# Optimization experiments

Hardware: AMD Instinct MI355X
Metric: run time of the kernel (lower is better)

## Reference

```python
import jax, jax.numpy as jnp
import numpy as np

C = 512      # filters
G = 32       # groups
EPS = 1e-6

def setup_inputs() -> dict:
    key = jax.random.key(0)
    ks = jax.random.split(key, 10)
    B, H, W = 2, 64, 64
    inputs = jax.random.normal(ks[0], (B, H, W, C), dtype=jnp.float32)
    scale = 1.0 / np.sqrt(C)
    def w(k):
        return jax.random.normal(k, (C, C), dtype=jnp.float32) * scale
    return {
        "inputs": inputs,
        "gn_gamma": jnp.ones((C,), jnp.float32),
        "gn_beta": jnp.zeros((C,), jnp.float32),
        "wq": w(ks[1]), "bq": jnp.zeros((C,), jnp.float32),
        "wk": w(ks[2]), "bk": jnp.zeros((C,), jnp.float32),
        "wv": w(ks[3]), "bv": jnp.zeros((C,), jnp.float32),
        "wo": w(ks[4]), "bo": jnp.zeros((C,), jnp.float32),
    }

def _group_norm(x, gamma, beta):
    B, H, W, c = x.shape
    xg = x.reshape(B, H, W, G, c // G)
    mean = jnp.mean(xg, axis=(1, 2, 4), keepdims=True)
    var = jnp.var(xg, axis=(1, 2, 4), keepdims=True)
    xg = (xg - mean) * jax.lax.rsqrt(var + EPS)
    return xg.reshape(B, H, W, c) * gamma + beta

def reference(inputs, gn_gamma, gn_beta, wq, bq, wk, bk, wv, bv, wo, bo):
    B, H, W, c = inputs.shape
    x = _group_norm(inputs, gn_gamma, gn_beta)
    # 1x1 convs == per-pixel linear layers
    q = (x @ wq + bq).reshape(B, H * W, c)
    k = (x @ wk + bk).reshape(B, H * W, c)
    v = (x @ wv + bv).reshape(B, H * W, c)
    q = q * jnp.asarray(1.0 / np.sqrt(float(c)), q.dtype)
    scores = jnp.einsum('bnc,bmc->bnm', q, k).astype(jnp.float32)  # [B,N,N]
    probs = jax.nn.softmax(scores, axis=-1).astype(inputs.dtype)
    attn = jnp.einsum('bnm,bmc->bnc', probs, v)
    out = attn.reshape(B, H, W, c) @ wo + bo
    return out + inputs
```

## Files before the change

### kernel.cpp

```cpp
#include <hip/hip_runtime.h>
#include <math.h>

typedef __bf16 bf16;
typedef __bf16 bf16x8 __attribute__((ext_vector_type(8)));
typedef float  f32x4  __attribute__((ext_vector_type(4)));

#define DEV __device__ __forceinline__
#define VMCNT(n) asm volatile("s_waitcnt vmcnt(" #n ")" ::: "memory")
#define CFENCE  asm volatile("" ::: "memory")
#define BAR()   { CFENCE; __builtin_amdgcn_s_barrier(); CFENCE; }

DEV void gload_lds16(const bf16* g, bf16* l) {
  __builtin_amdgcn_global_load_lds(
      (const __attribute__((address_space(1))) void*)g,
      (__attribute__((address_space(3))) void*)l, 16, 0, 0);
}

#define OFF_STATS 0UL
#define OFF_WOT   1024UL
#define OFF_BIASQ 525312UL
#define OFF_WTQKV 531456UL
#define OFF_XN    2104320UL
#define OFF_QKV   10492928UL
#define OFF_VT    35658752UL
#define OFF_S     44047360UL
#define OFF_INVL  111156224UL
#define OFF_P0    2104320UL
#define OFF_P1    18881536UL
#define OFF_ATTN  44047360UL
#define OFF_GNP   44047360UL

__global__ __launch_bounds__(256) void gn_part_k(const float* __restrict__ x,
                                                 float2* __restrict__ part) {
  const int blk = blockIdx.x;
  const int chunk = blk & 15;
  const int bg = blk >> 4;
  const int b = bg >> 5, g = bg & 31;
  const int t = threadIdx.x;
  const int p = chunk * 256 + t;
  const float* xp = x + (size_t)b * (4096 * 512) + (size_t)p * 512 + g * 16;
  float4 v0 = *(const float4*)(xp);
  float4 v1 = *(const float4*)(xp + 4);
  float4 v2 = *(const float4*)(xp + 8);
  float4 v3 = *(const float4*)(xp + 12);
  float s  = v0.x + v0.y + v0.z + v0.w + v1.x + v1.y + v1.z + v1.w
           + v2.x + v2.y + v2.z + v2.w + v3.x + v3.y + v3.z + v3.w;
  float ss = v0.x*v0.x + v0.y*v0.y + v0.z*v0.z + v0.w*v0.w
           + v1.x*v1.x + v1.y*v1.y + v1.z*v1.z + v1.w*v1.w
           + v2.x*v2.x + v2.y*v2.y + v2.z*v2.z + v2.w*v2.w
           + v3.x*v3.x + v3.y*v3.y + v3.z*v3.z + v3.w*v3.w;
#pragma unroll
  for (int off = 32; off; off >>= 1) {
    s  += __shfl_xor(s, off);
    ss += __shfl_xor(ss, off);
  }
  __shared__ float rs[4], rss[4];
  const int w = t >> 6, l = t & 63;
  if (l == 0) { rs[w] = s; rss[w] = ss; }
  __syncthreads();
  if (t == 0)
    part[blk] = make_float2(rs[0] + rs[1] + rs[2] + rs[3],
                            rss[0] + rss[1] + rss[2] + rss[3]);
}

__global__ void gn_finish_k(const float2* __restrict__ part,
                            float2* __restrict__ stats) {
  const int g = threadIdx.x;
  float s = 0.f, ss = 0.f;
#pragma unroll
  for (int c = 0; c < 16; ++c) {
    float2 p = part[g * 16 + c];
    s += p.x; ss += p.y;
  }
  float mean = s * (1.0f / 65536.0f);
  float var  = ss * (1.0f / 65536.0f) - mean * mean;
  stats[g] = make_float2(mean, 1.0f / sqrtf(var + 1e-6f));
}

__global__ __launch_bounds__(256) void gn_apply_k(const float* __restrict__ x,
                                                  const float2* __restrict__ stats,
                                                  const float* __restrict__ gamma,
                                                  const float* __restrict__ beta,
                                                  bf16* __restrict__ xn) {
  size_t i = ((size_t)blockIdx.x * 256 + threadIdx.x) * 8;
  const int c = (int)(i & 511);
  const int b = (int)(i >> 21);
  float2 st = stats[b * 32 + (c >> 4)];
  float4 xa = *(const float4*)(x + i);
  float4 xb = *(const float4*)(x + i + 4);
  float4 ga = *(const float4*)(gamma + c);
  float4 gb = *(const float4*)(gamma + c + 4);
  float4 ba = *(const float4*)(beta + c);
  float4 bb = *(const float4*)(beta + c + 4);
  bf16x8 o;
  o[0] = (bf16)((xa.x - st.x) * st.y * ga.x + ba.x);
  o[1] = (bf16)((xa.y - st.x) * st.y * ga.y + ba.y);
  o[2] = (bf16)((xa.z - st.x) * st.y * ga.z + ba.z);
  o[3] = (bf16)((xa.w - st.x) * st.y * ga.w + ba.w);
  o[4] = (bf16)((xb.x - st.x) * st.y * gb.x + bb.x);
  o[5] = (bf16)((xb.y - st.x) * st.y * gb.y + bb.y);
  o[6] = (bf16)((xb.z - st.x) * st.y * gb.z + bb.z);
  o[7] = (bf16)((xb.w - st.x) * st.y * gb.w + bb.w);
  *(bf16x8*)(xn + i) = o;
}

__global__ void prep_w_k(const float* __restrict__ wq, const float* __restrict__ wk,
                         const float* __restrict__ wv, const float* __restrict__ wo,
                         bf16* __restrict__ wt_qkv, bf16* __restrict__ wot, float qscale) {
  const int z = blockIdx.z;
  const float* W = (z == 0) ? wq : (z == 1) ? wk : (z == 2) ? wv : wo;
  bf16* dst = (z < 3) ? (wt_qkv + (size_t)z * 512 * 512) : wot;
  const float s = (z == 0) ? qscale : 1.0f;
  __shared__ float tile[32][33];
  const int i0 = blockIdx.y * 32;
  const int o0 = blockIdx.x * 32;
#pragma unroll
  for (int r = threadIdx.y; r < 32; r += 8)
    tile[r][threadIdx.x] = W[(size_t)(i0 + r) * 512 + o0 + threadIdx.x];
  __syncthreads();
#pragma unroll
  for (int r = threadIdx.y; r < 32; r += 8)
    dst[(size_t)(o0 + r) * 512 + i0 + threadIdx.x] = (bf16)(tile[threadIdx.x][r] * s);
}

__global__ void prep_bias_k(const float* __restrict__ bq, const float* __restrict__ bk,
                            const float* __restrict__ bv, float* __restrict__ bias_qkv,
                            float qscale) {
  int i = blockIdx.x * 256 + threadIdx.x;
  float v = (i < 512) ? bq[i] * qscale : (i < 1024) ? bk[i - 512] : bv[i - 1024];
  bias_qkv[i] = v;
}

__global__ void transpose_v_k(const bf16* __restrict__ qkv, bf16* __restrict__ vt) {
  __shared__ bf16 tile[32][33];
  const int z = blockIdx.z;
  const int n0 = blockIdx.x * 32, d0 = blockIdx.y * 32;
  const bf16* src = qkv + (size_t)z * 4096 * 1536 + 1024;
#pragma unroll
  for (int r = threadIdx.y; r < 32; r += 8)
    tile[r][threadIdx.x] = src[(size_t)(n0 + r) * 1536 + d0 + threadIdx.x];
  __syncthreads();
  bf16* dst = vt + (size_t)z * 512 * 4096;
#pragma unroll
  for (int r = threadIdx.y; r < 32; r += 8)
    dst[(size_t)(d0 + r) * 4096 + n0 + threadIdx.x] = tile[threadIdx.x][r];
}

__global__ __launch_bounds__(256) void rowsum_k(const bf16* __restrict__ S,
                                                float* __restrict__ invl) {
  const int r = blockIdx.x;
  const bf16* p = S + (size_t)r * 4096 + threadIdx.x * 16;
  bf16x8 u0 = *(const bf16x8*)p;
  bf16x8 u1 = *(const bf16x8*)(p + 8);
  float s = 0.f;
#pragma unroll
  for (int j = 0; j < 8; ++j) s += (float)u0[j] + (float)u1[j];
#pragma unroll
  for (int off = 32; off; off >>= 1) s += __shfl_xor(s, off);
  __shared__ float red[4];
  const int w = threadIdx.x >> 6, l = threadIdx.x & 63;
  if (l == 0) red[w] = s;
  __syncthreads();
  if (threadIdx.x == 0)
    invl[r] = 1.0f / (red[0] + red[1] + red[2] + red[3]);
}

__global__ __launch_bounds__(256) void reduce_pv_k(const float* __restrict__ p0,
                                                   const float* __restrict__ p1,
                                                   const float* __restrict__ invl,
                                                   bf16* __restrict__ attn) {
  size_t i = ((size_t)blockIdx.x * 256 + threadIdx.x) * 8;
  const float il = invl[i >> 9];
  float4 a = *(const float4*)(p0 + i);
  float4 b = *(const float4*)(p0 + i + 4);
  float4 c = *(const float4*)(p1 + i);
  float4 d = *(const float4*)(p1 + i + 4);
  bf16x8 o;
  o[0] = (bf16)((a.x + c.x) * il); o[1] = (bf16)((a.y + c.y) * il);
  o[2] = (bf16)((a.z + c.z) * il); o[3] = (bf16)((a.w + c.w) * il);
  o[4] = (bf16)((b.x + d.x) * il); o[5] = (bf16)((b.y + d.y) * il);
  o[6] = (bf16)((b.z + d.z) * il); o[7] = (bf16)((b.w + d.w) * il);
  *(bf16x8*)(attn + i) = o;
}

template <int BM, int BN, int EPI, int GX, int GY, int GZ>
__global__ __launch_bounds__(256, 2) void gemm_nt(
    const bf16* __restrict__ A, int lda, long sAz,
    const bf16* __restrict__ B, int ldb, long sBz,
    void* __restrict__ C, int ldc, long sCz,
    int nk,
    const float* __restrict__ bias,
    const float* __restrict__ resid) {
  constexpr int WM = BM / 2, WN = BN / 2;
  constexpr int FM = BM / 32, FN = BN / 32;
  constexpr int NWG = GX * GY * GZ;
  constexpr int CPX = NWG / 8;
  __shared__ alignas(16) bf16 As[2][BM * 64];
  __shared__ alignas(16) bf16 Bs[2][BN * 64];

  const int lin = blockIdx.x;
  const int wid = (lin & 7) * CPX + (lin >> 3);
  const int bx = wid % GX;
  const int by = (wid / GX) % GY;
  const int bz = wid / (GX * GY);

  const int t = threadIdx.x;
  const bf16* Aq = A + (size_t)bz * sAz + (size_t)by * BM * lda;
  const bf16* Bq = B + (size_t)bz * sBz + (size_t)bx * BN * ldb;

  const int srow = t >> 3;
  const int sg   = (t & 7) ^ (srow & 7);

  auto stage = [&](int buf, int kt) {
    const int k0 = kt * 64 + sg * 8;
#pragma unroll
    for (int i = 0; i < BM / 32; ++i)
      gload_lds16(Aq + (size_t)(i * 32 + srow) * lda + k0, &As[buf][i * 2048 + t * 8]);
#pragma unroll
    for (int i = 0; i < BN / 32; ++i)
      gload_lds16(Bq + (size_t)(i * 32 + srow) * ldb + k0, &Bs[buf][i * 2048 + t * 8]);
  };

  const int l = t & 63, w = t >> 6;
  const int wr = w >> 1, wc = w & 1;
  const int lr = l & 15, kh = l >> 4;
  const int rs = lr & 7;

  f32x4 acc[FM][FN] = {};

  stage(0, 0);
  for (int kt = 0; kt < nk; ++kt) {
    __syncthreads();
    if (kt + 1 < nk) stage((kt + 1) & 1, kt + 1);
    const int buf = kt & 1;
    bf16x8 a[2][FM], b[2][FN];
#pragma unroll
    for (int h = 0; h < 2; ++h) {
      const int g = ((h * 4 + kh) ^ rs) * 8;
#pragma unroll
      for (int m = 0; m < FM; ++m)
        a[h][m] = *(const bf16x8*)(&As[buf][(wr * WM + m * 16 + lr) * 64 + g]);
#pragma unroll
      for (int n = 0; n < FN; ++n)
        b[h][n] = *(const bf16x8*)(&Bs[buf][(wc * WN + n * 16 + lr) * 64 + g]);
    }
#pragma unroll
    for (int h = 0; h < 2; ++h)
#pragma unroll
      for (int m = 0; m < FM; ++m)
#pragma unroll
        for (int n = 0; n < FN; ++n)
          acc[m][n] = __builtin_amdgcn_mfma_f32_16x16x32_bf16(a[h][m], b[h][n], acc[m][n], 0, 0, 0);
  }

  const int gr0 = by * BM + wr * WM + kh * 4;
  const int gc0 = bx * BN + wc * WN + lr;
#pragma unroll
  for (int m = 0; m < FM; ++m)
#pragma unroll
    for (int n = 0; n < FN; ++n) {
      const int c = gc0 + n * 16;
      float bv = bias[c];
#pragma unroll
      for (int j = 0; j < 4; ++j) {
        const int r = gr0 + m * 16 + j;
        float val = acc[m][n][j] + bv;
        if constexpr (EPI == 2) {
          float* Cf = (float*)C + (size_t)bz * sCz;
          Cf[(size_t)r * ldc + c] = val + resid[(size_t)r * ldc + c];
        } else {
          bf16* Cb = (bf16*)C + (size_t)bz * sCz;
          Cb[(size_t)r * ldc + c] = (bf16)val;
        }
      }
    }
}

template <int BM, int BN, int WR, int WC, int EPI, int GX, int GY, int GZ, int KS>
__global__ __launch_bounds__(512, 2) void gemm_8p(
    const bf16* __restrict__ A, int lda, long sAz,
    const bf16* __restrict__ B, int ldb, long sBz,
    void* __restrict__ C0, void* __restrict__ C1, int ldc, long sCz,
    int nt) {
  constexpr int WM = BM / WR, WN = BN / WC;
  constexpr int FM = WM / 16, FN = WN / 16;
  constexpr int HM = FM / 2, HN = FN / 2;
  constexpr int LA = BM / 128, LB = BN / 128;
  constexpr int NWG = GX * KS * GY * GZ;
  constexpr int CPX = NWG / 8;
  static_assert(WR * WC == 8, "8 waves");
  static_assert(LA == 2 && (LB == 1 || LB == 2), "vmcnt literals");

  __shared__ alignas(16) bf16 As[2][BM * 64];
  __shared__ alignas(16) bf16 Bs[2][BN * 64];

  const int t = threadIdx.x;
  const int lin = blockIdx.x;
  const int wid = (lin & 7) * CPX + (lin >> 3);
  const int bx = wid % GX;
  const int ks = (wid / GX) % KS;
  const int by = (wid / (GX * KS)) % GY;
  const int bz = wid / (GX * KS * GY);

  const long kOff = (long)ks * nt * 64;
  const bf16* Aq = A + (size_t)bz * sAz + (size_t)by * BM * lda + kOff;
  const bf16* Bq = B + (size_t)bz * sBz + (size_t)bx * BN * ldb + kOff;

  const int srow = t >> 3;
  const int sgr  = (t & 7) ^ (srow & 7);

  auto stageA = [&](int buf, int tile, int half) {
    const bf16* src = Aq + (size_t)(half * (BM / 2) + srow) * lda + tile * 64 + sgr * 8;
    bf16* dst = &As[buf][(half * (BM / 2)) * 64] + t * 8;
#pragma unroll
    for (int j = 0; j < LA; ++j)
      gload_lds16(src + (size_t)(j * 64) * lda, dst + j * 4096);
  };
  auto stageB = [&](int buf, int tile, int half) {
    const bf16* src = Bq + (size_t)(half * (BN / 2) + srow) * ldb + tile * 64 + sgr * 8;
    bf16* dst = &Bs[buf][(half * (BN / 2)) * 64] + t * 8;
#pragma unroll
    for (int j = 0; j < LB; ++j)
      gload_lds16(src + (size_t)(j * 64) * ldb, dst + j * 4096);
  };

  const int l = t & 63, w = t >> 6;
  const int wr = w / WC, wc = w % WC;
  const int lr = l & 15, kh = l >> 4;
  const int rs8 = lr & 7;

  bf16x8 af[HM][2], bf_[HN][2];
  auto readA = [&](int buf, int qm) {
#pragma unroll
    for (int i = 0; i < HM; ++i)
#pragma unroll
      for (int h = 0; h < 2; ++h)
        af[i][h] = *(const bf16x8*)(
            &As[buf][(wr * WM + qm * (WM / 2) + i * 16 + lr) * 64 + (((h * 4 + kh) ^ rs8) * 8)]);
  };
  auto readB = [&](int buf, int qn) {
#pragma unroll
    for (int j = 0; j < HN; ++j)
#pragma unroll
      for (int h = 0; h < 2; ++h)
        bf_[j][h] = *(const bf16x8*)(
            &Bs[buf][(wc * WN + qn * (WN / 2) + j * 16 + lr) * 64 + (((h * 4 + kh) ^ rs8) * 8)]);
  };

  f32x4 acc[FM][FN] = {};

#define MFMAQ(QM, QN) { \
  __builtin_amdgcn_s_setprio(1); \
  _Pragma("unroll") for (int ii = 0; ii < HM; ++ii) \
  _Pragma("unroll") for (int jj = 0; jj < HN; ++jj) \
  _Pragma("unroll") for (int h = 0; h < 2; ++h) \
    acc[(QM)*HM + ii][(QN)*HN + jj] = __builtin_amdgcn_mfma_f32_16x16x32_bf16( \
        af[ii][h], bf_[jj][h], acc[(QM)*HM + ii][(QN)*HN + jj], 0, 0, 0); \
  __builtin_amdgcn_s_setprio(0); }
#define WAIT_LB() { if constexpr (LB == 1) VMCNT(1); else VMCNT(2); }

  stageA(0, 0, 0); stageA(0, 0, 1); stageB(0, 0, 0); stageB(0, 0, 1);
  WAIT_LB();
  BAR();

  const int half = nt >> 1;
  for (int i = 0; i < half; ++i) {
    const int t1 = 2 * i + 1, t2 = 2 * i + 2;
    const bool last = (i == half - 1);
    readA(0, 0); readB(0, 0);
    stageA(1, t1, 0);
    BAR();
    MFMAQ(0, 0);
    BAR();
    readA(0, 1);
    stageA(1, t1, 1);
    BAR();
    MFMAQ(1, 0);
    VMCNT(4);
    BAR();
    readB(0, 1);
    stageB(1, t1, 0);
    BAR();
    MFMAQ(1, 1);
    BAR();
    readA(0, 0);
    stageB(1, t1, 1);
    BAR();
    MFMAQ(0, 1);
    WAIT_LB();
    BAR();
    readA(1, 0); readB(1, 0);
    if (!last) stageA(0, t2, 0);
    BAR();
    MFMAQ(0, 0);
    BAR();
    readA(1, 1);
    if (!last) stageA(0, t2, 1);
    BAR();
    MFMAQ(1, 0);
    if (last) { VMCNT(0); } else { VMCNT(4); }
    BAR();
    readB(1, 1);
    if (!last) stageB(0, t2, 0);
    BAR();
    MFMAQ(1, 1);
    BAR();
    readA(1, 0);
    if (!last) stageB(0, t2, 1);
    BAR();
    MFMAQ(0, 1);
    WAIT_LB();
    BAR();
  }
#undef MFMAQ
#undef WAIT_LB

  const int gr0 = by * BM + wr * WM + kh * 4;
  const int gc0 = bx * BN + wc * WN + lr;
#pragma unroll
  for (int m = 0; m < FM; ++m)
#pragma unroll
    for (int n = 0; n < FN; ++n) {
      const int c = gc0 + n * 16;
#pragma unroll
      for (int j = 0; j < 4; ++j) {
        const int r = gr0 + m * 16 + j;
        if constexpr (EPI == 6) {
          bf16* Cb = (bf16*)C0 + (size_t)bz * sCz;
          Cb[(size_t)r * ldc + c] = (bf16)__expf(acc[m][n][j]);
        } else {
          float* Cf = (float*)(ks ? C1 : C0) + (size_t)bz * sCz;
          Cf[(size_t)r * ldc + c] = acc[m][n][j];
        }
      }
    }
}

extern "C" void kernel_launch(void* const* d_in, const int* in_sizes, int n_in,
                              void* d_out, int out_size, void* d_ws, size_t ws_size,
                              hipStream_t stream) {
  const float* x     = (const float*)d_in[0];
  const float* gamma = (const float*)d_in[1];
  const float* beta  = (const float*)d_in[2];
  const float* wq = (const float*)d_in[3];
  const float* bq = (const float*)d_in[4];
  const float* wk = (const float*)d_in[5];
  const float* bk = (const float*)d_in[6];
  const float* wv = (const float*)d_in[7];
  const float* bv = (const float*)d_in[8];
  const float* wo = (const float*)d_in[9];
  const float* bo = (const float*)d_in[10];
  float* out = (float*)d_out;
  char* ws = (char*)d_ws;

  float2* stats    = (float2*)(ws + OFF_STATS);
  bf16*   wot      = (bf16*)(ws + OFF_WOT);
  float*  bias_qkv = (float*)(ws + OFF_BIASQ);
  bf16*   wt_qkv   = (bf16*)(ws + OFF_WTQKV);
  bf16*   xn       = (bf16*)(ws + OFF_XN);
  bf16*   qkv      = (bf16*)(ws + OFF_QKV);
  bf16*   vt       = (bf16*)(ws + OFF_VT);
  bf16*   S        = (bf16*)(ws + OFF_S);
  float*  invl     = (float*)(ws + OFF_INVL);
  float*  p0       = (float*)(ws + OFF_P0);
  float*  p1       = (float*)(ws + OFF_P1);
  bf16*   attn     = (bf16*)(ws + OFF_ATTN);
  float2* gn_part  = (float2*)(ws + OFF_GNP);

  const float qscale = 0.04419417382415922f;

  prep_w_k<<<dim3(16, 16, 4), dim3(32, 8), 0, stream>>>(wq, wk, wv, wo, wt_qkv, wot, qscale);
  prep_bias_k<<<6, 256, 0, stream>>>(bq, bk, bv, bias_qkv, qscale);
  gn_part_k<<<1024, 256, 0, stream>>>(x, gn_part);
  gn_finish_k<<<1, 64, 0, stream>>>(gn_part, stats);
  gn_apply_k<<<2048, 256, 0, stream>>>(x, stats, gamma, beta, xn);

  gemm_nt<128, 128, 1, 12, 64, 1><<<768, 256, 0, stream>>>(
      xn, 512, 0, wt_qkv, 512, 0, qkv, 1536, 0, 512 / 64, bias_qkv, nullptr);

  gemm_8p<256, 256, 2, 4, 6, 16, 16, 2, 1><<<512, 512, 0, stream>>>(
      qkv, 1536, 4096L * 1536, qkv + 512, 1536, 4096L * 1536,
      S, nullptr, 4096, 4096L * 4096, 512 / 64);

  rowsum_k<<<8192, 256, 0, stream>>>(S, invl);

  transpose_v_k<<<dim3(128, 16, 2), dim3(32, 8), 0, stream>>>(qkv, vt);

  gemm_8p<256, 128, 4, 2, 3, 4, 16, 2, 2><<<256, 512, 0, stream>>>(
      S, 4096, 4096L * 4096, vt, 4096, 512L * 4096,
      p0, p1, 512, 4096L * 512, 2048 / 64);

  reduce_pv_k<<<2048, 256, 0, stream>>>(p0, p1, invl, attn);

  gemm_nt<64, 128, 2, 4, 128, 1><<<512, 256, 0, stream>>>(
      attn, 512, 0, wot, 512, 0, out, 512, 0, 512 / 64, bo, x);
}
```

Baseline: 165.1 us.

## Write V transposed from QKV GEMM epilogue and interleave 8-phase warp tiles

Splits the QKV projection into a QK GEMM and a separate V GEMM whose epilogue writes V directly in transposed layout with 4-wide bf16 stores. This removes the standalone transpose kernel and the round trip of V through global memory. It also changes the LDS read and output indexing in the 8-phase GEMM so each wave's quadrants are interleaved across block halves, which is meant to reduce LDS bank conflicts. The trade-off is one extra kernel launch and a smaller V GEMM grid that may fill the GPU poorly.

```diff
diff --git a/kernel.cpp b/kernel.cpp
--- a/kernel.cpp
+++ b/kernel.cpp
@@ -2,6 +2,7 @@
 #include <math.h>
 
 typedef __bf16 bf16;
+typedef __bf16 bf16x4 __attribute__((ext_vector_type(4)));
 typedef __bf16 bf16x8 __attribute__((ext_vector_type(8)));
 typedef float  f32x4  __attribute__((ext_vector_type(4)));
 
@@ -21,7 +22,7 @@
 #define OFF_BIASQ 525312UL
 #define OFF_WTQKV 531456UL
 #define OFF_XN    2104320UL
-#define OFF_QKV   10492928UL
+#define OFF_QK    10492928UL
 #define OFF_VT    35658752UL
 #define OFF_S     44047360UL
 #define OFF_INVL  111156224UL
@@ -131,21 +132,6 @@
   bias_qkv[i] = v;
 }
 
-__global__ void transpose_v_k(const bf16* __restrict__ qkv, bf16* __restrict__ vt) {
-  __shared__ bf16 tile[32][33];
-  const int z = blockIdx.z;
-  const int n0 = blockIdx.x * 32, d0 = blockIdx.y * 32;
-  const bf16* src = qkv + (size_t)z * 4096 * 1536 + 1024;
-#pragma unroll
-  for (int r = threadIdx.y; r < 32; r += 8)
-    tile[r][threadIdx.x] = src[(size_t)(n0 + r) * 1536 + d0 + threadIdx.x];
-  __syncthreads();
-  bf16* dst = vt + (size_t)z * 512 * 4096;
-#pragma unroll
-  for (int r = threadIdx.y; r < 32; r += 8)
-    dst[(size_t)(d0 + r) * 4096 + n0 + threadIdx.x] = tile[threadIdx.x][r];
-}
-
 __global__ __launch_bounds__(256) void rowsum_k(const bf16* __restrict__ S,
                                                 float* __restrict__ invl) {
   const int r = blockIdx.x;
@@ -261,16 +247,25 @@
     for (int n = 0; n < FN; ++n) {
       const int c = gc0 + n * 16;
       float bv = bias[c];
-#pragma unroll
-      for (int j = 0; j < 4; ++j) {
-        const int r = gr0 + m * 16 + j;
-        float val = acc[m][n][j] + bv;
-        if constexpr (EPI == 2) {
-          float* Cf = (float*)C + (size_t)bz * sCz;
-          Cf[(size_t)r * ldc + c] = val + resid[(size_t)r * ldc + c];
-        } else {
-          bf16* Cb = (bf16*)C + (size_t)bz * sCz;
-          Cb[(size_t)r * ldc + c] = (bf16)val;
+      if constexpr (EPI == 7) {
+        const int r0 = gr0 + m * 16;
+        const int z = r0 >> 12, nn = r0 & 4095;
+        bf16x4 v;
+#pragma unroll
+        for (int j = 0; j < 4; ++j) v[j] = (bf16)(acc[m][n][j] + bv);
+        *(bf16x4*)((bf16*)C + (size_t)z * (512 * 4096) + (size_t)c * 4096 + nn) = v;
+      } else {
+#pragma unroll
+        for (int j = 0; j < 4; ++j) {
+          const int r = gr0 + m * 16 + j;
+          float val = acc[m][n][j] + bv;
+          if constexpr (EPI == 2) {
+            float* Cf = (float*)C + (size_t)bz * sCz;
+            Cf[(size_t)r * ldc + c] = val + resid[(size_t)r * ldc + c];
+          } else {
+            bf16* Cb = (bf16*)C + (size_t)bz * sCz;
+            Cb[(size_t)r * ldc + c] = (bf16)val;
+          }
         }
       }
     }
@@ -336,7 +331,7 @@
 #pragma unroll
       for (int h = 0; h < 2; ++h)
         af[i][h] = *(const bf16x8*)(
-            &As[buf][(wr * WM + qm * (WM / 2) + i * 16 + lr) * 64 + (((h * 4 + kh) ^ rs8) * 8)]);
+            &As[buf][(qm * (BM / 2) + wr * (WM / 2) + i * 16 + lr) * 64 + (((h * 4 + kh) ^ rs8) * 8)]);
   };
   auto readB = [&](int buf, int qn) {
 #pragma unroll
@@ -344,7 +339,7 @@
 #pragma unroll
       for (int h = 0; h < 2; ++h)
         bf_[j][h] = *(const bf16x8*)(
-            &Bs[buf][(wc * WN + qn * (WN / 2) + j * 16 + lr) * 64 + (((h * 4 + kh) ^ rs8) * 8)]);
+            &Bs[buf][(qn * (BN / 2) + wc * (WN / 2) + j * 16 + lr) * 64 + (((h * 4 + kh) ^ rs8) * 8)]);
   };
 
   f32x4 acc[FM][FN] = {};
@@ -415,16 +410,17 @@
 #undef MFMAQ
 #undef WAIT_LB
 
-  const int gr0 = by * BM + wr * WM + kh * 4;
-  const int gc0 = bx * BN + wc * WN + lr;
+  const int gr0 = by * BM + wr * (WM / 2) + kh * 4;
+  const int gc0 = bx * BN + wc * (WN / 2) + lr;
 #pragma unroll
   for (int m = 0; m < FM; ++m)
 #pragma unroll
     for (int n = 0; n < FN; ++n) {
-      const int c = gc0 + n * 16;
+      const int c = gc0 + (n / HN) * (BN / 2) + (n % HN) * 16;
+      const int rb = gr0 + (m / HM) * (BM / 2) + (m % HM) * 16;
 #pragma unroll
       for (int j = 0; j < 4; ++j) {
-        const int r = gr0 + m * 16 + j;
+        const int r = rb + j;
         if constexpr (EPI == 6) {
           bf16* Cb = (bf16*)C0 + (size_t)bz * sCz;
           Cb[(size_t)r * ldc + c] = (bf16)__expf(acc[m][n][j]);
@@ -458,7 +454,7 @@
   float*  bias_qkv = (float*)(ws + OFF_BIASQ);
   bf16*   wt_qkv   = (bf16*)(ws + OFF_WTQKV);
   bf16*   xn       = (bf16*)(ws + OFF_XN);
-  bf16*   qkv      = (bf16*)(ws + OFF_QKV);
+  bf16*   qk       = (bf16*)(ws + OFF_QK);
   bf16*   vt       = (bf16*)(ws + OFF_VT);
   bf16*   S        = (bf16*)(ws + OFF_S);
   float*  invl     = (float*)(ws + OFF_INVL);
@@ -475,16 +471,18 @@
   gn_finish_k<<<1, 64, 0, stream>>>(gn_part, stats);
   gn_apply_k<<<2048, 256, 0, stream>>>(x, stats, gamma, beta, xn);
 
-  gemm_nt<128, 128, 1, 12, 64, 1><<<768, 256, 0, stream>>>(
-      xn, 512, 0, wt_qkv, 512, 0, qkv, 1536, 0, 512 / 64, bias_qkv, nullptr);
+  gemm_nt<128, 128, 1, 8, 64, 1><<<512, 256, 0, stream>>>(
+      xn, 512, 0, wt_qkv, 512, 0, qk, 1024, 0, 512 / 64, bias_qkv, nullptr);
+
+  gemm_nt<128, 128, 7, 4, 64, 1><<<256, 256, 0, stream>>>(
+      xn, 512, 0, wt_qkv + 1024 * 512, 512, 0, vt, 0, 0, 512 / 64,
+      bias_qkv + 1024, nullptr);
 
   gemm_8p<256, 256, 2, 4, 6, 16, 16, 2, 1><<<512, 512, 0, stream>>>(
-      qkv, 1536, 4096L * 1536, qkv + 512, 1536, 4096L * 1536,
+      qk, 1024, 4096L * 1024, qk + 512, 1024, 4096L * 1024,
       S, nullptr, 4096, 4096L * 4096, 512 / 64);
 
   rowsum_k<<<8192, 256, 0, stream>>>(S, invl);
-
-  transpose_v_k<<<dim3(128, 16, 2), dim3(32, 8), 0, stream>>>(qkv, vt);
 
   gemm_8p<256, 128, 4, 2, 3, 4, 16, 2, 2><<<256, 512, 0, stream>>>(
       S, 4096, 4096L * 4096, vt, 4096, 512L * 4096,
```

Result: slower. 170.1 us (+3.0%).
